# Performance work log

Hardware: AMD Instinct MI355X
Metric: run time of the kernel (lower is better)

## Reference

```python
import jax, jax.numpy as jnp
import numpy as np

# Flax nn.LSTMCell math: gates i,f,g,o; input dense has no bias, hidden dense has bias.
# We fuse the four gate projections into single [D,4H] / [H,4H] matrices in order (i,f,g,o).

def _lstm_layer(x, Wx, Wh, b):
    # x: [B,T,D], Wx: [D,4H], Wh: [H,4H], b: [4H]
    B = x.shape[0]
    H = Wh.shape[0]
    # Precompute input projections for the whole sequence (one big GEMM).
    xW = jnp.einsum('btd,dg->btg', x, Wx) + b  # [B,T,4H]

    def step(carry, xw_t):
        c, h = carry
        z = xw_t + h @ Wh  # [B,4H]
        i, f, g, o = jnp.split(z, 4, axis=-1)
        i = jax.nn.sigmoid(i)
        f = jax.nn.sigmoid(f)
        g = jnp.tanh(g)
        o = jax.nn.sigmoid(o)
        c = f * c + i * g
        h = o * jnp.tanh(c)
        return (c, h), h

    init = (jnp.zeros((B, H), x.dtype), jnp.zeros((B, H), x.dtype))
    _, ys = jax.lax.scan(step, init, jnp.swapaxes(xW, 0, 1))  # scan over T
    return jnp.swapaxes(ys, 0, 1)  # [B,T,H]


def setup_inputs() -> dict:
    key = jax.random.key(0)
    ks = jax.random.split(key, 7)
    B, T, D, H = 64, 512, 512, 1024
    s = lambda fan_in: 1.0 / np.sqrt(fan_in)
    x = jax.random.normal(ks[0], (B, T, D), dtype=jnp.float32)
    Wx0 = jax.random.normal(ks[1], (D, 4 * H), dtype=jnp.float32) * s(D)
    Wh0 = jax.random.normal(ks[2], (H, 4 * H), dtype=jnp.float32) * s(H)
    b0 = jnp.zeros((4 * H,), dtype=jnp.float32)
    Wx1 = jax.random.normal(ks[3], (H, 4 * H), dtype=jnp.float32) * s(H)
    Wh1 = jax.random.normal(ks[4], (H, 4 * H), dtype=jnp.float32) * s(H)
    b1 = jnp.zeros((4 * H,), dtype=jnp.float32)
    return {"x": x, "Wx0": Wx0, "Wh0": Wh0, "b0": b0, "Wx1": Wx1, "Wh1": Wh1, "b1": b1}


def reference(x, Wx0, Wh0, b0, Wx1, Wh1, b1):
    h1 = _lstm_layer(x, Wx0, Wh0, b0)
    h2 = _lstm_layer(h1, Wx1, Wh1, b1)
    return h2
```

## Files before the change

kernel.cpp:

```cpp
#include <hip/hip_runtime.h>

typedef __attribute__((ext_vector_type(8))) short short8;
typedef __attribute__((ext_vector_type(4))) float f32x4;

#define WS_XB     0ull
#define WS_W0T    33554432ull
#define WS_W1T    46137344ull
#define WS_RING0  62914560ull
#define WS_RING1  67108864ull
#define WS_BAR    71303168ull
#define SLOT_ELEMS 65536
#define SLOT_BYTES 131072

#define ARR0(g)  ((g) * 16)
#define ARR1(g)  (128 + (g) * 16)
#define ROOT0    256
#define ROOT1    272
#define POLL0(g) (288 + (g) * 16)
#define POLL1(g) (416 + (g) * 16)

__device__ __forceinline__ unsigned short f2bf(float f) {
  unsigned u = __float_as_uint(f);
  u += 0x7FFFu + ((u >> 16) & 1u);
  return (unsigned short)(u >> 16);
}

__device__ __forceinline__ float sigm(float x) { return 1.0f / (1.0f + __expf(-x)); }

__global__ void sentinel_kernel(float* out) { out[0] = 1.0e6f; }

__global__ void convert_x_kernel(const float* __restrict__ x, unsigned short* __restrict__ xb) {
  int i = blockIdx.x * 256 + threadIdx.x;
  const float4 v = ((const float4*)x)[i];
  unsigned long long pack = (unsigned long long)f2bf(v.x)
                          | ((unsigned long long)f2bf(v.y) << 16)
                          | ((unsigned long long)f2bf(v.z) << 32)
                          | ((unsigned long long)f2bf(v.w) << 48);
  ((unsigned long long*)xb)[i] = pack;
}

__global__ void transpose_weights_kernel(const float* __restrict__ wx, const float* __restrict__ wh,
                                         unsigned short* __restrict__ dst, int Kx, int Ktot) {
  __shared__ float tile[32][33];
  const int k0 = blockIdx.x * 32, n0 = blockIdx.y * 32;
  const int tx = threadIdx.x, ty = threadIdx.y;
#pragma unroll
  for (int i = 0; i < 4; ++i) {
    int k = k0 + ty + i * 8;
    tile[ty + i * 8][tx] = (k < Kx) ? wx[(size_t)k * 4096 + n0 + tx]
                                    : wh[(size_t)(k - Kx) * 4096 + n0 + tx];
  }
  __syncthreads();
#pragma unroll
  for (int i = 0; i < 4; ++i) {
    int n = n0 + ty + i * 8;
    int r = (n & 1023) * 4 + (n >> 10);
    dst[(size_t)r * Ktot + k0 + tx] = f2bf(tile[tx][ty + i * 8]);
  }
}

template<int N1, int NBLK>
__device__ __forceinline__ void lstm_step_mfma(int a0b, int a1b,
    const unsigned short* __restrict__ r1p, const unsigned short* __restrict__ r2p,
    f32x4& acc0, f32x4& acc1)
{
  extern __shared__ unsigned short lds[];
  short8 buf[4][8];

  auto loadB = [&](int slot, int blk) {
    const unsigned short* p = (blk < N1) ? (r1p + blk * 256) : (r2p + (blk - N1) * 256);
#pragma unroll
    for (int j = 0; j < 8; ++j) buf[slot][j] = *(const short8*)(p + j * 32);
  };
  auto compute8 = [&](int slot, int kg) {
#pragma unroll
    for (int j = 0; j < 8; ++j) {
      const int ko = kg + j * 32;
      short8 a0 = *(const short8*)&lds[a0b + ko];
      short8 a1 = *(const short8*)&lds[a1b + ko];
      acc0 = __builtin_amdgcn_mfma_f32_16x16x32_bf16(a0, buf[slot][j], acc0, 0, 0, 0);
      acc1 = __builtin_amdgcn_mfma_f32_16x16x32_bf16(a1, buf[slot][j], acc1, 0, 0, 0);
    }
  };

  loadB(0, 0); loadB(1, 1); loadB(2, 2); loadB(3, 3);
  __builtin_amdgcn_sched_barrier(0);
#pragma unroll
  for (int bp = 0; bp < NBLK; ++bp) {
    compute8(bp & 3, bp * 256);
    if (bp + 4 < NBLK) loadB(bp & 3, bp + 4);
    __builtin_amdgcn_sched_barrier(0);
  }
}

__global__ void __launch_bounds__(256, 1) lstm_persistent(
    const unsigned short* __restrict__ xb,
    const unsigned short* __restrict__ w0t,
    const unsigned short* __restrict__ w1t,
    const float* __restrict__ b0v, const float* __restrict__ b1v,
    unsigned short* __restrict__ ring0, unsigned short* __restrict__ ring1,
    unsigned* __restrict__ bar,
    float* __restrict__ out)
{
  extern __shared__ unsigned short lds[];

  const int wg    = blockIdx.x;
  const int group = wg >> 7;
  const int wgl   = wg & 127;
  const int hu0   = wgl * 8;
  const int tid   = threadIdx.x;
  const int lane  = tid & 63;
  const int wid   = tid >> 6;
  const int c16   = lane & 15;
  const int row4  = lane >> 4;
  const int bb    = wid * 16 + c16;

  const int K    = group ? 2048 : 1536;
  const int KPAD = group ? 2056 : 1544;

  {
    const unsigned short* wsrc = (group ? w1t : w0t) + (size_t)(wgl * 32) * K;
    const int kv = K >> 3;
    for (int c = tid; c < 32 * kv; c += 256) {
      int r = c / kv, q = c - r * kv;
      int srcr = 8 * ((r & 15) >> 2) + 4 * (r >> 4) + (r & 3);
      *(short8*)&lds[r * KPAD + q * 8] = *(const short8*)&wsrc[(size_t)srcr * K + q * 8];
    }
  }
  __syncthreads();

  const float* bsrc = group ? b1v : b0v;
  float bias0[4], bias1[4];
#pragma unroll
  for (int j = 0; j < 4; ++j) {
    bias0[j] = bsrc[j * 1024 + hu0 + 2 * row4];
    bias1[j] = bsrc[j * 1024 + hu0 + 2 * row4 + 1];
  }

  const int a0b = c16 * KPAD + 8 * row4;
  const int a1b = a0b + 16 * KPAD;

  const int lofs = (bb << 10) + 8 * row4;
  const unsigned short* x_cur = xb + ((size_t)bb << 18) + 8 * row4;
  unsigned* rwb0 = (unsigned*)(group ? ring1 : ring0) + (((bb << 10) + hu0) >> 1);
  float* out_base = out + ((size_t)bb << 19) + hu0 + 2 * row4;

  const int grp = wgl >> 4;
  unsigned* arrw  = bar + (group ? ARR1(grp) : ARR0(grp));
  unsigned* rootw = bar + (group ? ROOT1 : ROOT0);
  unsigned long long* pollw =
      (unsigned long long*)(bar + (group ? POLL1(grp) : POLL0(grp)));

  float cst0 = 0.0f, cst1 = 0.0f;

  auto compute_episode = [&](int s) {
    const int t = group ? (s - 1) : s;

    f32x4 acc0 = { bias0[0], bias0[1], bias0[2], bias0[3] };
    f32x4 acc1 = { bias1[0], bias1[1], bias1[2], bias1[3] };

    const unsigned short* h0rd = ring0 + ((s - 1) & 31) * SLOT_ELEMS + lofs;
    if (group == 0) {
      lstm_step_mfma<2, 6>(a0b, a1b, x_cur, h0rd, acc0, acc1);
      x_cur += 512;
    } else {
      const unsigned short* h1rd = ring1 + ((s - 2) & 31) * SLOT_ELEMS + lofs;
      lstm_step_mfma<4, 8>(a0b, a1b, h0rd, h1rd, acc0, acc1);
    }

    float hv0, hv1;
    {
      float iv = sigm(acc0[0]), fv = sigm(acc0[1]);
      float gv = tanhf(acc0[2]), ov = sigm(acc0[3]);
      cst0 = fv * cst0 + iv * gv;
      hv0 = ov * tanhf(cst0);
    }
    {
      float iv = sigm(acc1[0]), fv = sigm(acc1[1]);
      float gv = tanhf(acc1[2]), ov = sigm(acc1[3]);
      cst1 = fv * cst1 + iv * gv;
      hv1 = ov * tanhf(cst1);
    }
    unsigned hp  = (unsigned)f2bf(hv0) | ((unsigned)f2bf(hv1) << 16);
    unsigned hpo = __shfl_down(hp, 16);
    if ((row4 & 1) == 0) {
      unsigned long long pk = (unsigned long long)hp | ((unsigned long long)hpo << 32);
      unsigned long long* dst = (unsigned long long*)(rwb0 + (t & 31) * (SLOT_ELEMS / 2) + row4);
      __hip_atomic_store(dst, pk, __ATOMIC_RELAXED, __HIP_MEMORY_SCOPE_AGENT);
    }
    if (group) {
      float2 o2; o2.x = hv0; o2.y = hv1;
      *(float2*)(out_base + ((size_t)t << 10)) = o2;
    }
  };

  for (int s = 0; s < 512; ++s) {
    const bool active = group ? (s >= 1) : true;
    if (active) compute_episode(s);

    __syncthreads();
    if (tid == 0) {
      unsigned old = __hip_atomic_fetch_add(arrw, 1u, __ATOMIC_RELAXED, __HIP_MEMORY_SCOPE_AGENT);
      if (old == (unsigned)(16 * s + 15)) {
        unsigned old2 = __hip_atomic_fetch_add(rootw, 1u, __ATOMIC_RELAXED, __HIP_MEMORY_SCOPE_AGENT);
        if (old2 == (unsigned)(8 * s + 7)) {
#pragma unroll
          for (int g2 = 0; g2 < 8; ++g2) {
            (void)__hip_atomic_exchange(bar + (group ? POLL1(g2) : POLL0(g2)), (unsigned)(s + 1),
                                        __ATOMIC_RELAXED, __HIP_MEMORY_SCOPE_AGENT);
            (void)__hip_atomic_exchange(bar + (group ? POLL0(g2) : POLL1(g2)) + 1, (unsigned)(s + 1),
                                        __ATOMIC_RELAXED, __HIP_MEMORY_SCOPE_AGENT);
          }
        }
      }
      const int own_tgt = s + 1;
      const int mir_tgt = group ? (s + 1) : (s - 3);
      for (;;) {
        unsigned long long v = __hip_atomic_load(pollw, __ATOMIC_RELAXED, __HIP_MEMORY_SCOPE_AGENT);
        int rel = (int)(unsigned)v;
        int mir = (int)(unsigned)(v >> 32);
        if (rel >= own_tgt && mir >= mir_tgt) break;
        __builtin_amdgcn_s_sleep(1);
      }
    }
    __syncthreads();
  }
  if (group) compute_episode(512);
}

extern "C" void kernel_launch(void* const* d_in, const int* in_sizes, int n_in,
                              void* d_out, int out_size, void* d_ws, size_t ws_size,
                              hipStream_t stream) {
  const float* x   = (const float*)d_in[0];
  const float* Wx0 = (const float*)d_in[1];
  const float* Wh0 = (const float*)d_in[2];
  const float* b0  = (const float*)d_in[3];
  const float* Wx1 = (const float*)d_in[4];
  const float* Wh1 = (const float*)d_in[5];
  const float* b1  = (const float*)d_in[6];
  float* outp = (float*)d_out;

  char* ws = (char*)d_ws;
  unsigned short* xbp   = (unsigned short*)(ws + WS_XB);
  unsigned short* w0tp  = (unsigned short*)(ws + WS_W0T);
  unsigned short* w1tp  = (unsigned short*)(ws + WS_W1T);
  unsigned short* ring0 = (unsigned short*)(ws + WS_RING0);
  unsigned short* ring1 = (unsigned short*)(ws + WS_RING1);
  unsigned*       barp  = (unsigned*)(ws + WS_BAR);

  sentinel_kernel<<<dim3(1), dim3(1), 0, stream>>>(outp);
  convert_x_kernel<<<dim3(16384), dim3(256), 0, stream>>>(x, xbp);
  transpose_weights_kernel<<<dim3(48, 128), dim3(32, 8), 0, stream>>>(Wx0, Wh0, w0tp, 512, 1536);
  transpose_weights_kernel<<<dim3(64, 128), dim3(32, 8), 0, stream>>>(Wx1, Wh1, w1tp, 1024, 2048);
  hipMemsetAsync(ring0 + 31 * SLOT_ELEMS, 0, SLOT_BYTES, stream);
  hipMemsetAsync(ring1 + 31 * SLOT_ELEMS, 0, SLOT_BYTES, stream);
  hipMemsetAsync(barp, 0, 4096, stream);

  void* kargs[] = { (void*)&xbp, (void*)&w0tp, (void*)&w1tp, (void*)&b0, (void*)&b1,
                    (void*)&ring0, (void*)&ring1, (void*)&barp, (void*)&outp };
  hipError_t e = hipLaunchCooperativeKernel((void*)lstm_persistent, dim3(256), dim3(256),
                                            kargs, 32 * 2056 * 2 , stream);
  if (e != hipSuccess) {
    lstm_persistent<<<dim3(256), dim3(256), 32 * 2056 * 2, stream>>>(
        xbp, w0tp, w1tp, b0, b1, ring0, ring1, barp, outp);
  }
}
```

Baseline: 4.858 ms.

## Split LSTM persistent kernel across 512 workgroups with half the hidden units each

Doubles the workgroup count of the persistent LSTM kernel from 256 to 512, so each workgroup owns 4 hidden units (16 weight rows) instead of 8, with one MFMA accumulator chain per wave instead of two. Weight LDS footprint is halved and launch bounds allow two workgroups per CU, which spreads the per-step recurrent GEMM across more CUs/waves. The barrier tree grows to 16 groups per layer, and each step now has more participants, more atomics and more polling. Each wave also still streams the full B operand (h and x) from global for only half the MFMA work, which doubles redundant load traffic.

```diff
diff --git a/kernel.cpp b/kernel.cpp
--- a/kernel.cpp
+++ b/kernel.cpp
@@ -13,11 +13,11 @@
 #define SLOT_BYTES 131072
 
 #define ARR0(g)  ((g) * 16)
-#define ARR1(g)  (128 + (g) * 16)
-#define ROOT0    256
-#define ROOT1    272
-#define POLL0(g) (288 + (g) * 16)
-#define POLL1(g) (416 + (g) * 16)
+#define ARR1(g)  (256 + (g) * 16)
+#define ROOT0    512
+#define ROOT1    528
+#define POLL0(g) (544 + (g) * 16)
+#define POLL1(g) (800 + (g) * 16)
 
 __device__ __forceinline__ unsigned short f2bf(float f) {
   unsigned u = __float_as_uint(f);
@@ -60,9 +60,9 @@
 }
 
 template<int N1, int NBLK>
-__device__ __forceinline__ void lstm_step_mfma(int a0b, int a1b,
+__device__ __forceinline__ void lstm_step_mfma(int a0b,
     const unsigned short* __restrict__ r1p, const unsigned short* __restrict__ r2p,
-    f32x4& acc0, f32x4& acc1)
+    f32x4& acc0)
 {
   extern __shared__ unsigned short lds[];
   short8 buf[4][8];
@@ -77,9 +77,7 @@
     for (int j = 0; j < 8; ++j) {
       const int ko = kg + j * 32;
       short8 a0 = *(const short8*)&lds[a0b + ko];
-      short8 a1 = *(const short8*)&lds[a1b + ko];
       acc0 = __builtin_amdgcn_mfma_f32_16x16x32_bf16(a0, buf[slot][j], acc0, 0, 0, 0);
-      acc1 = __builtin_amdgcn_mfma_f32_16x16x32_bf16(a1, buf[slot][j], acc1, 0, 0, 0);
     }
   };
 
@@ -93,7 +91,7 @@
   }
 }
 
-__global__ void __launch_bounds__(256, 1) lstm_persistent(
+__global__ void __launch_bounds__(256, 2) lstm_persistent(
     const unsigned short* __restrict__ xb,
     const unsigned short* __restrict__ w0t,
     const unsigned short* __restrict__ w1t,
@@ -105,9 +103,9 @@
   extern __shared__ unsigned short lds[];
 
   const int wg    = blockIdx.x;
-  const int group = wg >> 7;
-  const int wgl   = wg & 127;
-  const int hu0   = wgl * 8;
+  const int group = wg >> 8;
+  const int wgl   = wg & 255;
+  const int hu0   = wgl * 4;
   const int tid   = threadIdx.x;
   const int lane  = tid & 63;
   const int wid   = tid >> 6;
@@ -119,31 +117,26 @@
   const int KPAD = group ? 2056 : 1544;
 
   {
-    const unsigned short* wsrc = (group ? w1t : w0t) + (size_t)(wgl * 32) * K;
+    const unsigned short* wsrc = (group ? w1t : w0t) + (size_t)(wgl * 16) * K;
     const int kv = K >> 3;
-    for (int c = tid; c < 32 * kv; c += 256) {
+    for (int c = tid; c < 16 * kv; c += 256) {
       int r = c / kv, q = c - r * kv;
-      int srcr = 8 * ((r & 15) >> 2) + 4 * (r >> 4) + (r & 3);
-      *(short8*)&lds[r * KPAD + q * 8] = *(const short8*)&wsrc[(size_t)srcr * K + q * 8];
+      *(short8*)&lds[r * KPAD + q * 8] = *(const short8*)&wsrc[(size_t)r * K + q * 8];
     }
   }
   __syncthreads();
 
   const float* bsrc = group ? b1v : b0v;
-  float bias0[4], bias1[4];
-#pragma unroll
-  for (int j = 0; j < 4; ++j) {
-    bias0[j] = bsrc[j * 1024 + hu0 + 2 * row4];
-    bias1[j] = bsrc[j * 1024 + hu0 + 2 * row4 + 1];
-  }
+  float bias[4];
+#pragma unroll
+  for (int j = 0; j < 4; ++j) bias[j] = bsrc[j * 1024 + hu0 + row4];
 
   const int a0b = c16 * KPAD + 8 * row4;
-  const int a1b = a0b + 16 * KPAD;
 
   const int lofs = (bb << 10) + 8 * row4;
   const unsigned short* x_cur = xb + ((size_t)bb << 18) + 8 * row4;
-  unsigned* rwb0 = (unsigned*)(group ? ring1 : ring0) + (((bb << 10) + hu0) >> 1);
-  float* out_base = out + ((size_t)bb << 19) + hu0 + 2 * row4;
+  unsigned short* rwb = (group ? ring1 : ring0) + (bb << 10) + hu0;
+  float* out_base = out + ((size_t)bb << 19) + hu0 + row4;
 
   const int grp = wgl >> 4;
   unsigned* arrw  = bar + (group ? ARR1(grp) : ARR0(grp));
@@ -151,47 +144,36 @@
   unsigned long long* pollw =
       (unsigned long long*)(bar + (group ? POLL1(grp) : POLL0(grp)));
 
-  float cst0 = 0.0f, cst1 = 0.0f;
+  float cst = 0.0f;
 
   auto compute_episode = [&](int s) {
     const int t = group ? (s - 1) : s;
 
-    f32x4 acc0 = { bias0[0], bias0[1], bias0[2], bias0[3] };
-    f32x4 acc1 = { bias1[0], bias1[1], bias1[2], bias1[3] };
+    f32x4 acc0 = { bias[0], bias[1], bias[2], bias[3] };
 
     const unsigned short* h0rd = ring0 + ((s - 1) & 31) * SLOT_ELEMS + lofs;
     if (group == 0) {
-      lstm_step_mfma<2, 6>(a0b, a1b, x_cur, h0rd, acc0, acc1);
+      lstm_step_mfma<2, 6>(a0b, x_cur, h0rd, acc0);
       x_cur += 512;
     } else {
       const unsigned short* h1rd = ring1 + ((s - 2) & 31) * SLOT_ELEMS + lofs;
-      lstm_step_mfma<4, 8>(a0b, a1b, h0rd, h1rd, acc0, acc1);
-    }
-
-    float hv0, hv1;
-    {
-      float iv = sigm(acc0[0]), fv = sigm(acc0[1]);
-      float gv = tanhf(acc0[2]), ov = sigm(acc0[3]);
-      cst0 = fv * cst0 + iv * gv;
-      hv0 = ov * tanhf(cst0);
-    }
-    {
-      float iv = sigm(acc1[0]), fv = sigm(acc1[1]);
-      float gv = tanhf(acc1[2]), ov = sigm(acc1[3]);
-      cst1 = fv * cst1 + iv * gv;
-      hv1 = ov * tanhf(cst1);
-    }
-    unsigned hp  = (unsigned)f2bf(hv0) | ((unsigned)f2bf(hv1) << 16);
-    unsigned hpo = __shfl_down(hp, 16);
-    if ((row4 & 1) == 0) {
-      unsigned long long pk = (unsigned long long)hp | ((unsigned long long)hpo << 32);
-      unsigned long long* dst = (unsigned long long*)(rwb0 + (t & 31) * (SLOT_ELEMS / 2) + row4);
+      lstm_step_mfma<4, 8>(a0b, h0rd, h1rd, acc0);
+    }
+
+    float iv = sigm(acc0[0]), fv = sigm(acc0[1]);
+    float gv = tanhf(acc0[2]), ov = sigm(acc0[3]);
+    cst = fv * cst + iv * gv;
+    float hv = ov * tanhf(cst);
+
+    unsigned hp = (unsigned)f2bf(hv);
+    unsigned lo = hp | (__shfl_down(hp, 16) << 16);
+    unsigned hi = __shfl_down(lo, 32);
+    if (row4 == 0) {
+      unsigned long long pk = (unsigned long long)lo | ((unsigned long long)hi << 32);
+      unsigned long long* dst = (unsigned long long*)(rwb + (t & 31) * SLOT_ELEMS);
       __hip_atomic_store(dst, pk, __ATOMIC_RELAXED, __HIP_MEMORY_SCOPE_AGENT);
     }
-    if (group) {
-      float2 o2; o2.x = hv0; o2.y = hv1;
-      *(float2*)(out_base + ((size_t)t << 10)) = o2;
-    }
+    if (group) out_base[(size_t)t << 10] = hv;
   };
 
   for (int s = 0; s < 512; ++s) {
@@ -203,9 +185,9 @@
       unsigned old = __hip_atomic_fetch_add(arrw, 1u, __ATOMIC_RELAXED, __HIP_MEMORY_SCOPE_AGENT);
       if (old == (unsigned)(16 * s + 15)) {
         unsigned old2 = __hip_atomic_fetch_add(rootw, 1u, __ATOMIC_RELAXED, __HIP_MEMORY_SCOPE_AGENT);
-        if (old2 == (unsigned)(8 * s + 7)) {
-#pragma unroll
-          for (int g2 = 0; g2 < 8; ++g2) {
+        if (old2 == (unsigned)(16 * s + 15)) {
+#pragma unroll
+          for (int g2 = 0; g2 < 16; ++g2) {
             (void)__hip_atomic_exchange(bar + (group ? POLL1(g2) : POLL0(g2)), (unsigned)(s + 1),
                                         __ATOMIC_RELAXED, __HIP_MEMORY_SCOPE_AGENT);
             (void)__hip_atomic_exchange(bar + (group ? POLL0(g2) : POLL1(g2)) + 1, (unsigned)(s + 1),
@@ -254,14 +236,14 @@
   transpose_weights_kernel<<<dim3(64, 128), dim3(32, 8), 0, stream>>>(Wx1, Wh1, w1tp, 1024, 2048);
   hipMemsetAsync(ring0 + 31 * SLOT_ELEMS, 0, SLOT_BYTES, stream);
   hipMemsetAsync(ring1 + 31 * SLOT_ELEMS, 0, SLOT_BYTES, stream);
-  hipMemsetAsync(barp, 0, 4096, stream);
+  hipMemsetAsync(barp, 0, 8192, stream);
 
   void* kargs[] = { (void*)&xbp, (void*)&w0tp, (void*)&w1tp, (void*)&b0, (void*)&b1,
                     (void*)&ring0, (void*)&ring1, (void*)&barp, (void*)&outp };
-  hipError_t e = hipLaunchCooperativeKernel((void*)lstm_persistent, dim3(256), dim3(256),
-                                            kargs, 32 * 2056 * 2 , stream);
+  hipError_t e = hipLaunchCooperativeKernel((void*)lstm_persistent, dim3(512), dim3(256),
+                                            kargs, 16 * 2056 * 2 , stream);
   if (e != hipSuccess) {
-    lstm_persistent<<<dim3(256), dim3(256), 32 * 2056 * 2, stream>>>(
+    lstm_persistent<<<dim3(512), dim3(256), 16 * 2056 * 2, stream>>>(
         xbp, w0tp, w1tp, b0, b1, ring0, ring1, barp, outp);
   }
 }
```

Result: slower. 7.564 ms (+55.7%).
